# Optimization experiments

Measured on AMD Instinct MI355X. Metric: run time of the kernel, lower is better.

Reference implementation:

```python
import jax, jax.numpy as jnp
import numpy as np

B, T, D, H, V, NPOS, NDEP, OUT = 65536, 7, 100, 700, 32000, 50, 45, 93


def setup_inputs() -> dict:
    key = jax.random.key(0)
    ks = jax.random.split(key, 16)
    word_idx = jax.random.randint(ks[0], (B, T), 0, V, dtype=jnp.int64)
    drop = jax.random.uniform(ks[1], (B, T)) < 0.05
    word_idx = jnp.where(drop, -1, word_idx)
    pos_idx = jax.random.randint(ks[2], (B, T), 0, NPOS, dtype=jnp.int32)
    dep_idx = jax.random.randint(ks[3], (B, T), 0, NDEP, dtype=jnp.int32)
    s = 0.05
    return {
        "word_idx": word_idx,
        "pos_idx": pos_idx,
        "dep_idx": dep_idx,
        "word_table": jax.random.normal(ks[4], (V, D), jnp.float32) * s,
        "pos_table": jax.random.normal(ks[5], (NPOS, D), jnp.float32) * s,
        "dep_table": jax.random.normal(ks[6], (NDEP, D), jnp.float32) * s,
        "Ww": jax.random.normal(ks[7], (T * D, H), jnp.float32) * s,
        "bw": jax.random.normal(ks[8], (H,), jnp.float32) * s,
        "Wp": jax.random.normal(ks[9], (T * D, H), jnp.float32) * s,
        "bp": jax.random.normal(ks[10], (H,), jnp.float32) * s,
        "Wd": jax.random.normal(ks[11], (T * D, H), jnp.float32) * s,
        "bd": jax.random.normal(ks[12], (H,), jnp.float32) * s,
        "Wo": jax.random.normal(ks[13], (H, OUT), jnp.float32) * s,
        "bo": jax.random.normal(ks[14], (OUT,), jnp.float32) * s,
    }


def reference(word_idx, pos_idx, dep_idx, word_table, pos_table, dep_table,
              Ww, bw, Wp, bp, Wd, bd, Wo, bo):
    b = word_idx.shape[0]
    # word lookup with -1 -> zeros (the '_' token), batched gather instead of
    # per-token loop + serial torch.cat
    we = jnp.where((word_idx >= 0)[..., None],
                   word_table[jnp.clip(word_idx, 0)], 0.0)          # [B,T,D]
    we = we.reshape(b, -1)                                           # [B,700]
    pe = pos_table[pos_idx].reshape(b, -1)                           # [B,700]
    de = dep_table[dep_idx].reshape(b, -1)                           # [B,700]
    h = (we @ Ww + bw) + (pe @ Wp + bp) + (de @ Wd + bd)             # [B,700]
    h = h * h * h                                                    # torch.pow(., 3)
    logits = h @ Wo + bo                                             # [B,OUT]
    # original applies Softmax(dim=0) to a 1-D [OUT] vector per example;
    # batched equivalent is softmax over the class axis
    return jax.nn.softmax(logits, axis=-1)
```

## Files before the change

kernel.cpp:

```cpp
#include <hip/hip_runtime.h>
#include <hip/hip_bf16.h>
#include <stdint.h>

#define T_ 7
#define D_ 100
#define KP 704
#define KSTEPS 22
#define NP 704
#define NT 44
#define BM 64
#define OUTC 93
#define OUTP 96
#define NT2 6
#define NPOS 50
#define NDEP 45

typedef __attribute__((ext_vector_type(8))) short bf16x8;
typedef __attribute__((ext_vector_type(4))) float f32x4;

#define SZ_WWP (22*44*64*8*2)
#define O_WWP  0
#define O_WOP  (O_WWP + SZ_WWP)
#define SZ_WOP (22*6*64*8*2)
#define O_PTB  (O_WOP + SZ_WOP)
#define SZ_PTB (7*50*704*2)
#define O_DTB  (O_PTB + SZ_PTB)
#define SZ_DTB (7*45*704*2)
#define O_HB   (O_DTB + SZ_DTB)

__device__ __forceinline__ unsigned short f2bf(float f) {
  unsigned u = __float_as_uint(f);
  u += 0x7FFFu + ((u >> 16) & 1u);
  return (unsigned short)(u >> 16);
}
__device__ __forceinline__ float bf2f(unsigned short h) {
  return __uint_as_float(((unsigned)h) << 16);
}
__device__ __forceinline__ void addbf8(float* s, const uint4 v) {
  unsigned u0 = v.x, u1 = v.y, u2 = v.z, u3 = v.w;
  s[0] += __uint_as_float(u0 << 16);
  s[1] += __uint_as_float(u0 & 0xFFFF0000u);
  s[2] += __uint_as_float(u1 << 16);
  s[3] += __uint_as_float(u1 & 0xFFFF0000u);
  s[4] += __uint_as_float(u2 << 16);
  s[5] += __uint_as_float(u2 & 0xFFFF0000u);
  s[6] += __uint_as_float(u3 << 16);
  s[7] += __uint_as_float(u3 & 0xFFFF0000u);
}

__global__ void pack_w(const float* __restrict__ W, unsigned short* __restrict__ out,
                       int Ksrc, int Nsrc, int ntiles) {
  int blk = blockIdx.x;
  int ks = blk / ntiles, nt = blk - ks*ntiles;
  int l = threadIdx.x;
  int n = nt*16 + (l & 15);
  int k0 = ks*32 + (l >> 4)*8;
  unsigned short v[8];
#pragma unroll
  for (int j = 0; j < 8; ++j) {
    int k = k0 + j;
    float f = (k < Ksrc && n < Nsrc) ? W[k*Nsrc + n] : 0.f;
    v[j] = f2bf(f);
  }
  ((uint4*)out)[blk*64 + l] = *(const uint4*)v;
}

__global__ void pack_tbl(const float* __restrict__ tbl, const float* __restrict__ W,
                         unsigned short* __restrict__ out, int P, int total) {
  int id = blockIdx.x*256 + threadIdx.x;
  if (id >= total) return;
  int hp = id % 704;
  int tp = id / 704;
  int p = tp % P, t = tp / P;
  float acc = 0.f;
  if (hp < 700) {
    const float* tr = tbl + p*100;
    const float* wc = W + t*100*700 + hp;
#pragma unroll 4
    for (int d = 0; d < 100; ++d) acc += tr[d] * wc[d*700];
  }
  out[id] = f2bf(acc);
}

__global__ void bias_sum(const float* __restrict__ a, const float* __restrict__ b,
                         const float* __restrict__ c, float* __restrict__ o) {
  int i = blockIdx.x*256 + threadIdx.x;
  if (i < 704) o[i] = (i < 700) ? (a[i] + b[i] + c[i]) : 0.f;
}

struct SMem {
  union {
    struct { unsigned short A[2][4*64*8]; unsigned short Bb[2][44*64*8]; } mm;
    struct { unsigned short h3[64*712]; float logits[64*96]; } ep;
  } u;
  int widx[64][8];
  int pidxs[64][8];
  int didxs[64][8];
  float bo_l[96];
};

__launch_bounds__(512, 2)
__global__ void dp_main(const int* __restrict__ word_idx,
                        const int* __restrict__ pos_idx,
                        const int* __restrict__ dep_idx,
                        const float* __restrict__ word_table,
                        const unsigned short* __restrict__ WwP,
                        const unsigned short* __restrict__ WoP,
                        const unsigned short* __restrict__ PTb,
                        const unsigned short* __restrict__ DTb,
                        const float* __restrict__ hbias,
                        const float* __restrict__ bo,
                        float* __restrict__ out) {
  __shared__ SMem sm;
  const int tid = threadIdx.x;
  const int lane = tid & 63;
  const int w = tid >> 6;
  const int blockRow = blockIdx.x * BM;

  if (tid < 448) {
    int r = tid / 7, t = tid - r*7;
    int g = (blockRow + r)*7 + t;
    sm.widx[r][t]  = word_idx[g];
    sm.pidxs[r][t] = pos_idx[g];
    sm.didxs[r][t] = dep_idx[g];
  }
  if (tid < 96) sm.bo_l[tid] = (tid < OUTC) ? bo[tid] : 0.f;

  f32x4 acc0[11], acc1[11];
#pragma unroll
  for (int j = 0; j < 11; ++j) { acc0[j] = (f32x4){0,0,0,0}; acc1[j] = (f32x4){0,0,0,0}; }

  __syncthreads();

  auto issueB = [&](int ks, int buf) {
    const unsigned short* src = WwP + (size_t)ks*(44*64*8);
    unsigned short* dst = sm.u.mm.Bb[buf];
#pragma unroll
    for (int it = 0; it < 6; ++it) {
      int slot = it*512 + tid;
      if (slot < 44*64) {
        __builtin_amdgcn_global_load_lds(
            (const __attribute__((address_space(1))) unsigned int*)(src + slot*8),
            (__attribute__((address_space(3))) unsigned int*)(dst + slot*8),
            16, 0, 0);
      }
    }
  };
  auto gatherA = [&](int ks, float4& fa, float4& fb) {
    int mt = tid >> 6;
    int l = tid & 63;
    int row = mt*16 + (l & 15);
    int k0 = ks*32 + (l >> 4)*8;
    int t0 = k0 / 100, d0 = k0 - t0*100;
    fa = make_float4(0.f,0.f,0.f,0.f);
    fb = make_float4(0.f,0.f,0.f,0.f);
    {
      int wi = sm.widx[row][t0];
      if (wi >= 0) fa = *(const float4*)(word_table + (size_t)wi*100 + d0);
    }
    int k4 = k0 + 4; int t1 = k4 / 100, d1 = k4 - t1*100;
    if (t1 < 7) {
      int wi = sm.widx[row][t1];
      if (wi >= 0) fb = *(const float4*)(word_table + (size_t)wi*100 + d1);
    }
  };
  auto writeA = [&](int buf, float4 fa, float4 fb) {
    unsigned short v[8];
    v[0]=f2bf(fa.x); v[1]=f2bf(fa.y); v[2]=f2bf(fa.z); v[3]=f2bf(fa.w);
    v[4]=f2bf(fb.x); v[5]=f2bf(fb.y); v[6]=f2bf(fb.z); v[7]=f2bf(fb.w);
    ((uint4*)sm.u.mm.A[buf])[tid] = *(const uint4*)v;
  };
  const int mtb = (w >> 2) * 2;
  const int ntb = (w & 3) * 11;
  auto compute = [&](int buf) {
    const bf16x8* Af = (const bf16x8*)sm.u.mm.A[buf];
    const bf16x8* Bf = (const bf16x8*)sm.u.mm.Bb[buf];
    bf16x8 a0 = Af[(mtb + 0)*64 + lane];
    bf16x8 a1 = Af[(mtb + 1)*64 + lane];
#pragma unroll
    for (int j = 0; j < 11; ++j) {
      bf16x8 b = Bf[(ntb + j)*64 + lane];
      acc0[j] = __builtin_amdgcn_mfma_f32_16x16x32_bf16(a0, b, acc0[j], 0, 0, 0);
      acc1[j] = __builtin_amdgcn_mfma_f32_16x16x32_bf16(a1, b, acc1[j], 0, 0, 0);
    }
  };

  issueB(0, 0);
  if (tid < 256) {
    float4 fa, fb;
    gatherA(0, fa, fb);
    writeA(0, fa, fb);
  }
  __syncthreads();

  int buf = 0;
  for (int ks = 0; ks < KSTEPS; ++ks) {
    float4 na, nb;
    const bool pre = (ks + 1 < KSTEPS);
    if (pre) {
      issueB(ks + 1, buf ^ 1);
      if (tid < 256) gatherA(ks + 1, na, nb);
    }
    compute(buf);
    if (pre && tid < 256) writeA(buf ^ 1, na, nb);
    __syncthreads();
    buf ^= 1;
  }

  {
    unsigned short* h3 = sm.u.ep.h3;
#pragma unroll 1
    for (int it = 0; it < 11; ++it) {
      int v = it*512 + tid;
      int row = v / 88;
      int c8 = v - row*88;
      int cb = c8*8;
      float s0[8];
      float4 hb0 = *(const float4*)(hbias + cb);
      float4 hb1 = *(const float4*)(hbias + cb + 4);
      s0[0]=hb0.x; s0[1]=hb0.y; s0[2]=hb0.z; s0[3]=hb0.w;
      s0[4]=hb1.x; s0[5]=hb1.y; s0[6]=hb1.z; s0[7]=hb1.w;
#pragma unroll
      for (int t = 0; t < 7; ++t) {
        int p = sm.pidxs[row][t];
        addbf8(s0, *(const uint4*)(PTb + ((size_t)(t*NPOS + p))*704 + cb));
        int dd = sm.didxs[row][t];
        addbf8(s0, *(const uint4*)(DTb + ((size_t)(t*NDEP + dd))*704 + cb));
      }
      unsigned short o[8];
#pragma unroll
      for (int j = 0; j < 8; ++j) o[j] = f2bf(s0[j]);
      *(uint4*)(h3 + row*712 + cb) = *(const uint4*)o;
    }
  }
  __syncthreads();

  {
    unsigned short* h3 = sm.u.ep.h3;
    const int lr = (lane >> 4)*4, lc = lane & 15;
#pragma unroll
    for (int j = 0; j < 11; ++j) {
      int col = (ntb + j)*16 + lc;
      {
        int rb = (mtb + 0)*16 + lr;
#pragma unroll
        for (int r = 0; r < 4; ++r) {
          int off = (rb + r)*712 + col;
          float h = acc0[j][r] + bf2f(h3[off]);
          h3[off] = f2bf(h*h*h);
        }
      }
      {
        int rb = (mtb + 1)*16 + lr;
#pragma unroll
        for (int r = 0; r < 4; ++r) {
          int off = (rb + r)*712 + col;
          float h = acc1[j][r] + bf2f(h3[off]);
          h3[off] = f2bf(h*h*h);
        }
      }
    }
  }
  __syncthreads();

  {
    const unsigned short* h3 = sm.u.ep.h3;
    int mt = w >> 1;
    int nb2 = (w & 1)*3;
    f32x4 c2[3];
#pragma unroll
    for (int jn = 0; jn < 3; ++jn) c2[jn] = (f32x4){0,0,0,0};
    const bf16x8* WoF = (const bf16x8*)WoP;
    bf16x8 bfr[3];
#pragma unroll
    for (int jn = 0; jn < 3; ++jn) bfr[jn] = WoF[(size_t)(nb2 + jn)*64 + lane];
    const int arow = mt*16 + (lane & 15);
    const int koff = (lane >> 4)*8;
    for (int ks = 0; ks < KSTEPS; ++ks) {
      bf16x8 a = *(const bf16x8*)(h3 + arow*712 + ks*32 + koff);
      bf16x8 bn[3];
      if (ks < KSTEPS-1) {
#pragma unroll
        for (int jn = 0; jn < 3; ++jn) bn[jn] = WoF[((size_t)(ks+1)*6 + nb2 + jn)*64 + lane];
      }
#pragma unroll
      for (int jn = 0; jn < 3; ++jn)
        c2[jn] = __builtin_amdgcn_mfma_f32_16x16x32_bf16(a, bfr[jn], c2[jn], 0, 0, 0);
      if (ks < KSTEPS-1) {
#pragma unroll
        for (int jn = 0; jn < 3; ++jn) bfr[jn] = bn[jn];
      }
    }
    float* lg = sm.u.ep.logits;
    const int lr = (lane >> 4)*4, lc = lane & 15;
#pragma unroll
    for (int jn = 0; jn < 3; ++jn)
#pragma unroll
      for (int r = 0; r < 4; ++r)
        lg[(mt*16 + lr + r)*96 + (nb2 + jn)*16 + lc] = c2[jn][r];
  }
  __syncthreads();

  {
    const float* lg = sm.u.ep.logits;
    int row = tid >> 3, s = tid & 7;
    const float4* lp = (const float4*)(lg + row*96 + s*12);
    float4 xa = lp[0], xb = lp[1], xc = lp[2];
    float x[12] = {xa.x,xa.y,xa.z,xa.w, xb.x,xb.y,xb.z,xb.w, xc.x,xc.y,xc.z,xc.w};
    int cb = s*12;
    float mx = -1e30f;
#pragma unroll
    for (int i = 0; i < 12; ++i) {
      int c = cb + i;
      x[i] += sm.bo_l[c];
      mx = fmaxf(mx, (c < OUTC) ? x[i] : -1e30f);
    }
    mx = fmaxf(mx, __shfl_xor(mx, 1, 8));
    mx = fmaxf(mx, __shfl_xor(mx, 2, 8));
    mx = fmaxf(mx, __shfl_xor(mx, 4, 8));
    float e[12]; float sum = 0.f;
#pragma unroll
    for (int i = 0; i < 12; ++i) {
      int c = cb + i;
      e[i] = (c < OUTC) ? __expf(x[i] - mx) : 0.f;
      sum += e[i];
    }
    sum += __shfl_xor(sum, 1, 8);
    sum += __shfl_xor(sum, 2, 8);
    sum += __shfl_xor(sum, 4, 8);
    float inv = 1.0f / sum;
    float* op = out + (size_t)(blockRow + row)*OUTC;
#pragma unroll
    for (int i = 0; i < 12; ++i) {
      int c = cb + i;
      if (c < OUTC) op[c] = e[i]*inv;
    }
  }
}

extern "C" void kernel_launch(void* const* d_in, const int* in_sizes, int n_in,
                              void* d_out, int out_size, void* d_ws, size_t ws_size,
                              hipStream_t stream) {
  const int*   word_idx   = (const int*)d_in[0];
  const int*   pos_idx    = (const int*)d_in[1];
  const int*   dep_idx    = (const int*)d_in[2];
  const float* word_table = (const float*)d_in[3];
  const float* pos_table  = (const float*)d_in[4];
  const float* dep_table  = (const float*)d_in[5];
  const float* Ww = (const float*)d_in[6];
  const float* bw = (const float*)d_in[7];
  const float* Wp = (const float*)d_in[8];
  const float* bp = (const float*)d_in[9];
  const float* Wd = (const float*)d_in[10];
  const float* bd = (const float*)d_in[11];
  const float* Wo = (const float*)d_in[12];
  const float* bo = (const float*)d_in[13];
  float* out = (float*)d_out;

  char* ws = (char*)d_ws;
  unsigned short* WwP   = (unsigned short*)(ws + O_WWP);
  unsigned short* WoP   = (unsigned short*)(ws + O_WOP);
  unsigned short* PTb   = (unsigned short*)(ws + O_PTB);
  unsigned short* DTb   = (unsigned short*)(ws + O_DTB);
  float*          hbias = (float*)(ws + O_HB);

  pack_w<<<22*44, 64, 0, stream>>>(Ww, WwP, 700, 700, 44);
  pack_w<<<22*6,  64, 0, stream>>>(Wo, WoP, 700, OUTC, 6);
  pack_tbl<<<(7*50*704 + 255)/256, 256, 0, stream>>>(pos_table, Wp, PTb, 50, 7*50*704);
  pack_tbl<<<(7*45*704 + 255)/256, 256, 0, stream>>>(dep_table, Wd, DTb, 45, 7*45*704);
  bias_sum<<<3, 256, 0, stream>>>(bw, bp, bd, hbias);
  dp_main<<<65536/BM, 512, 0, stream>>>(word_idx, pos_idx, dep_idx, word_table,
                                        WwP, WoP, PTb, DTb, hbias, bo, out);
}
```

Baseline: 307.2 us.

## Fold pos/dep tables and bias into one-hot extended GEMM K dimension

Adds the pos/dep lookups and the bias to the main GEMM as one-hot columns. K grows from 704 to 1376, and a concatenated weight matrix is built that holds Ww, the precomputed table×W products and a bias row. This removes the separate bf16 gather-add epilogue. It also switches to single-buffered LDS with two barriers per step, shrinks the h3 buffer by processing the second GEMM in two column halves, compacts index storage, and raises launch bounds to 4 blocks per CU. The cost is nearly double the MFMA work in the first GEMM and less overlap of loads with compute.

Result: slower. 333.2 us (+8.4%).

```diff
diff --git a/kernel.cpp b/kernel.cpp
--- a/kernel.cpp
+++ b/kernel.cpp
@@ -1,51 +1,26 @@
 #include <hip/hip_runtime.h>
-#include <hip/hip_bf16.h>
 #include <stdint.h>
 
-#define T_ 7
-#define D_ 100
-#define KP 704
-#define KSTEPS 22
-#define NP 704
-#define NT 44
 #define BM 64
+#define NTT 44
+#define KSTEPS 43
+#define KE 1376
+#define H3S 360
 #define OUTC 93
-#define OUTP 96
-#define NT2 6
-#define NPOS 50
-#define NDEP 45
+#define KS2 22
 
 typedef __attribute__((ext_vector_type(8))) short bf16x8;
 typedef __attribute__((ext_vector_type(4))) float f32x4;
 
-#define SZ_WWP (22*44*64*8*2)
-#define O_WWP  0
-#define O_WOP  (O_WWP + SZ_WWP)
-#define SZ_WOP (22*6*64*8*2)
-#define O_PTB  (O_WOP + SZ_WOP)
-#define SZ_PTB (7*50*704*2)
-#define O_DTB  (O_PTB + SZ_PTB)
-#define SZ_DTB (7*45*704*2)
-#define O_HB   (O_DTB + SZ_DTB)
+#define O_WB   0
+#define SZ_WB  (KSTEPS*NTT*64*8*2)
+#define O_WOP  (O_WB + SZ_WB)
+#define SZ_WOP (KS2*6*64*8*2)
 
 __device__ __forceinline__ unsigned short f2bf(float f) {
   unsigned u = __float_as_uint(f);
   u += 0x7FFFu + ((u >> 16) & 1u);
   return (unsigned short)(u >> 16);
-}
-__device__ __forceinline__ float bf2f(unsigned short h) {
-  return __uint_as_float(((unsigned)h) << 16);
-}
-__device__ __forceinline__ void addbf8(float* s, const uint4 v) {
-  unsigned u0 = v.x, u1 = v.y, u2 = v.z, u3 = v.w;
-  s[0] += __uint_as_float(u0 << 16);
-  s[1] += __uint_as_float(u0 & 0xFFFF0000u);
-  s[2] += __uint_as_float(u1 << 16);
-  s[3] += __uint_as_float(u1 & 0xFFFF0000u);
-  s[4] += __uint_as_float(u2 << 16);
-  s[5] += __uint_as_float(u2 & 0xFFFF0000u);
-  s[6] += __uint_as_float(u3 << 16);
-  s[7] += __uint_as_float(u3 & 0xFFFF0000u);
 }
 
 __global__ void pack_w(const float* __restrict__ W, unsigned short* __restrict__ out,
@@ -54,7 +29,7 @@
   int ks = blk / ntiles, nt = blk - ks*ntiles;
   int l = threadIdx.x;
   int n = nt*16 + (l & 15);
-  int k0 = ks*32 + (l >> 4)*8;
+  int k0 = ks*32 + ((l >> 4) << 3);
   unsigned short v[8];
 #pragma unroll
   for (int j = 0; j < 8; ++j) {
@@ -65,50 +40,68 @@
   ((uint4*)out)[blk*64 + l] = *(const uint4*)v;
 }
 
-__global__ void pack_tbl(const float* __restrict__ tbl, const float* __restrict__ W,
-                         unsigned short* __restrict__ out, int P, int total) {
-  int id = blockIdx.x*256 + threadIdx.x;
-  if (id >= total) return;
-  int hp = id % 704;
-  int tp = id / 704;
-  int p = tp % P, t = tp / P;
-  float acc = 0.f;
-  if (hp < 700) {
-    const float* tr = tbl + p*100;
-    const float* wc = W + t*100*700 + hp;
+__global__ void build_WB(const float* __restrict__ Ww, const float* __restrict__ Wp,
+                         const float* __restrict__ Wd, const float* __restrict__ pos_table,
+                         const float* __restrict__ dep_table, const float* __restrict__ bw,
+                         const float* __restrict__ bp, const float* __restrict__ bd,
+                         unsigned short* __restrict__ out) {
+  int blk = blockIdx.x;
+  int ks = blk / 11, q = blk - ks*11;
+  int l = threadIdx.x & 63;
+  int nt = q*4 + (threadIdx.x >> 6);
+  int n = nt*16 + (l & 15);
+  int k0 = ks*32 + ((l >> 4) << 3);
+  unsigned short v[8];
+#pragma unroll
+  for (int j = 0; j < 8; ++j) {
+    int k = k0 + j;
+    float val = 0.f;
+    if (n < 700) {
+      if (k < 700) {
+        val = Ww[k*700 + n];
+      } else if (k < 1050) {
+        int u = k - 700; int t = u/50; int p = u - t*50;
+        const float* tr = pos_table + p*100;
+        const float* wc = Wp + (t*100)*700 + n;
+        float a = 0.f;
 #pragma unroll 4
-    for (int d = 0; d < 100; ++d) acc += tr[d] * wc[d*700];
-  }
-  out[id] = f2bf(acc);
-}
-
-__global__ void bias_sum(const float* __restrict__ a, const float* __restrict__ b,
-                         const float* __restrict__ c, float* __restrict__ o) {
-  int i = blockIdx.x*256 + threadIdx.x;
-  if (i < 704) o[i] = (i < 700) ? (a[i] + b[i] + c[i]) : 0.f;
+        for (int d = 0; d < 100; ++d) a += tr[d] * wc[d*700];
+        val = a;
+      } else if (k < 1365) {
+        int u = k - 1050; int t = u/45; int dd = u - t*45;
+        const float* tr = dep_table + dd*100;
+        const float* wc = Wd + (t*100)*700 + n;
+        float a = 0.f;
+#pragma unroll 4
+        for (int d = 0; d < 100; ++d) a += tr[d] * wc[d*700];
+        val = a;
+      } else if (k == 1365) {
+        val = bw[n] + bp[n] + bd[n];
+      }
+    }
+    v[j] = f2bf(val);
+  }
+  ((uint4*)out)[(ks*NTT + nt)*64 + l] = *(const uint4*)v;
 }
 
 struct SMem {
   union {
-    struct { unsigned short A[2][4*64*8]; unsigned short Bb[2][44*64*8]; } mm;
-    struct { unsigned short h3[64*712]; float logits[64*96]; } ep;
+    struct { unsigned short A[4*64*8]; unsigned short B[NTT*64*8]; } mm;
+    unsigned short h3h[64*H3S];
   } u;
-  int widx[64][8];
-  int pidxs[64][8];
-  int didxs[64][8];
+  unsigned short widx[64][8];
+  unsigned char  pidx[64][8];
+  unsigned char  didx[64][8];
   float bo_l[96];
 };
 
-__launch_bounds__(512, 2)
+__launch_bounds__(512, 4)
 __global__ void dp_main(const int* __restrict__ word_idx,
                         const int* __restrict__ pos_idx,
                         const int* __restrict__ dep_idx,
                         const float* __restrict__ word_table,
-                        const unsigned short* __restrict__ WwP,
+                        const unsigned short* __restrict__ WB,
                         const unsigned short* __restrict__ WoP,
-                        const unsigned short* __restrict__ PTb,
-                        const unsigned short* __restrict__ DTb,
-                        const float* __restrict__ hbias,
                         const float* __restrict__ bo,
                         float* __restrict__ out) {
   __shared__ SMem sm;
@@ -120,61 +113,81 @@
   if (tid < 448) {
     int r = tid / 7, t = tid - r*7;
     int g = (blockRow + r)*7 + t;
-    sm.widx[r][t]  = word_idx[g];
-    sm.pidxs[r][t] = pos_idx[g];
-    sm.didxs[r][t] = dep_idx[g];
+    int wi = word_idx[g];
+    sm.widx[r][t] = (wi < 0) ? 0xFFFFu : (unsigned short)wi;
+    sm.pidx[r][t] = (unsigned char)pos_idx[g];
+    sm.didx[r][t] = (unsigned char)dep_idx[g];
   }
   if (tid < 96) sm.bo_l[tid] = (tid < OUTC) ? bo[tid] : 0.f;
 
+  const int amt   = tid >> 7;
+  const int alane = (tid >> 1) & 63;
+  const int ahalf = tid & 1;
+  const int arow  = amt*16 + (alane & 15);
+  const int ak    = ((alane >> 4) << 3) + ahalf*4;
+
+  const int mtb = (w >> 2) * 2;
+  const int ntb = (w & 3) * 11;
+
   f32x4 acc0[11], acc1[11];
 #pragma unroll
   for (int j = 0; j < 11; ++j) { acc0[j] = (f32x4){0,0,0,0}; acc1[j] = (f32x4){0,0,0,0}; }
 
-  __syncthreads();
-
-  auto issueB = [&](int ks, int buf) {
-    const unsigned short* src = WwP + (size_t)ks*(44*64*8);
-    unsigned short* dst = sm.u.mm.Bb[buf];
+  auto issueB = [&](int ks) {
+    const unsigned short* src = WB + (size_t)ks*(NTT*64*8);
 #pragma unroll
     for (int it = 0; it < 6; ++it) {
       int slot = it*512 + tid;
-      if (slot < 44*64) {
+      if (slot < NTT*64) {
         __builtin_amdgcn_global_load_lds(
             (const __attribute__((address_space(1))) unsigned int*)(src + slot*8),
-            (__attribute__((address_space(3))) unsigned int*)(dst + slot*8),
+            (__attribute__((address_space(3))) unsigned int*)(sm.u.mm.B + slot*8),
             16, 0, 0);
       }
     }
   };
-  auto gatherA = [&](int ks, float4& fa, float4& fb) {
-    int mt = tid >> 6;
-    int l = tid & 63;
-    int row = mt*16 + (l & 15);
-    int k0 = ks*32 + (l >> 4)*8;
-    int t0 = k0 / 100, d0 = k0 - t0*100;
-    fa = make_float4(0.f,0.f,0.f,0.f);
-    fb = make_float4(0.f,0.f,0.f,0.f);
-    {
-      int wi = sm.widx[row][t0];
-      if (wi >= 0) fa = *(const float4*)(word_table + (size_t)wi*100 + d0);
-    }
-    int k4 = k0 + 4; int t1 = k4 / 100, d1 = k4 - t1*100;
-    if (t1 < 7) {
-      int wi = sm.widx[row][t1];
-      if (wi >= 0) fb = *(const float4*)(word_table + (size_t)wi*100 + d1);
+  auto stage1 = [&](int ks, float4& g) {
+    int k0 = ks*32 + ak;
+    g = make_float4(0.f, 0.f, 0.f, 0.f);
+    if (k0 < 700) {
+      int t = k0/100, d = k0 - t*100;
+      unsigned wi = sm.widx[arow][t];
+      if (wi != 0xFFFFu) g = *(const float4*)(word_table + (size_t)wi*100 + d);
+    } else {
+      unsigned short r_[4];
+#pragma unroll
+      for (int j = 0; j < 4; ++j) {
+        int k = k0 + j;
+        unsigned short rv = 0;
+        if (k < 1050) {
+          int u = k - 700; int t = u/50; int pp = u - t*50;
+          if (pp == (int)sm.pidx[arow][t]) rv = 0x3F80;
+        } else if (k < 1365) {
+          int u = k - 1050; int t = u/45; int dd = u - t*45;
+          if (dd == (int)sm.didx[arow][t]) rv = 0x3F80;
+        } else if (k == 1365) rv = 0x3F80;
+        r_[j] = rv;
+      }
+      g.x = __uint_as_float((unsigned)r_[0] | ((unsigned)r_[1] << 16));
+      g.y = __uint_as_float((unsigned)r_[2] | ((unsigned)r_[3] << 16));
     }
   };
-  auto writeA = [&](int buf, float4 fa, float4 fb) {
-    unsigned short v[8];
-    v[0]=f2bf(fa.x); v[1]=f2bf(fa.y); v[2]=f2bf(fa.z); v[3]=f2bf(fa.w);
-    v[4]=f2bf(fb.x); v[5]=f2bf(fb.y); v[6]=f2bf(fb.z); v[7]=f2bf(fb.w);
-    ((uint4*)sm.u.mm.A[buf])[tid] = *(const uint4*)v;
+  auto stage2 = [&](int ks, float4 g) {
+    int k0 = ks*32 + ak;
+    unsigned v0, v1;
+    if (k0 < 700) {
+      v0 = (unsigned)f2bf(g.x) | ((unsigned)f2bf(g.y) << 16);
+      v1 = (unsigned)f2bf(g.z) | ((unsigned)f2bf(g.w) << 16);
+    } else {
+      v0 = __float_as_uint(g.x);
+      v1 = __float_as_uint(g.y);
+    }
+    uint2 pk; pk.x = v0; pk.y = v1;
+    *(uint2*)(sm.u.mm.A + ((amt*64 + alane)*8 + ahalf*4)) = pk;
   };
-  const int mtb = (w >> 2) * 2;
-  const int ntb = (w & 3) * 11;
-  auto compute = [&](int buf) {
-    const bf16x8* Af = (const bf16x8*)sm.u.mm.A[buf];
-    const bf16x8* Bf = (const bf16x8*)sm.u.mm.Bb[buf];
+  auto compute = [&]() {
+    const bf16x8* Af = (const bf16x8*)sm.u.mm.A;
+    const bf16x8* Bf = (const bf16x8*)sm.u.mm.B;
     bf16x8 a0 = Af[(mtb + 0)*64 + lane];
     bf16x8 a1 = Af[(mtb + 1)*64 + lane];
 #pragma unroll
@@ -185,124 +198,74 @@
     }
   };
 
-  issueB(0, 0);
-  if (tid < 256) {
-    float4 fa, fb;
-    gatherA(0, fa, fb);
-    writeA(0, fa, fb);
-  }
+  issueB(0);
   __syncthreads();
-
-  int buf = 0;
+  {
+    float4 g; stage1(0, g); stage2(0, g);
+  }
+  __syncthreads();
+
   for (int ks = 0; ks < KSTEPS; ++ks) {
-    float4 na, nb;
+    float4 gn;
     const bool pre = (ks + 1 < KSTEPS);
-    if (pre) {
-      issueB(ks + 1, buf ^ 1);
-      if (tid < 256) gatherA(ks + 1, na, nb);
-    }
-    compute(buf);
-    if (pre && tid < 256) writeA(buf ^ 1, na, nb);
+    if (pre) stage1(ks + 1, gn);
+    compute();
     __syncthreads();
-    buf ^= 1;
+    if (pre) { issueB(ks + 1); stage2(ks + 1, gn); }
+    __syncthreads();
+  }
+
+  f32x4 c2[3];
+#pragma unroll
+  for (int jn = 0; jn < 3; ++jn) c2[jn] = (f32x4){0,0,0,0};
+  const int mt2 = w >> 1;
+  const int nb2 = (w & 1)*3;
+  const int arow2 = mt2*16 + (lane & 15);
+  const int koff2 = (lane >> 4)*8;
+  const bf16x8* WoF = (const bf16x8*)WoP;
+  const int myph = (w & 3) >> 1;
+  const int lr = ((lane >> 4) << 2), lc = lane & 15;
+
+#pragma unroll
+  for (int ph = 0; ph < 2; ++ph) {
+    if (myph == ph) {
+      int cbase = ntb*16 - ph*352;
+#pragma unroll
+      for (int j = 0; j < 11; ++j) {
+#pragma unroll
+        for (int r = 0; r < 4; ++r) {
+          float h0 = acc0[j][r];
+          float h1 = acc1[j][r];
+          sm.u.h3h[((mtb+0)*16 + lr + r)*H3S + cbase + j*16 + lc] = f2bf(h0*h0*h0);
+          sm.u.h3h[((mtb+1)*16 + lr + r)*H3S + cbase + j*16 + lc] = f2bf(h1*h1*h1);
+        }
+      }
+    }
+    __syncthreads();
+#pragma unroll 2
+    for (int ksl = 0; ksl < 11; ++ksl) {
+      bf16x8 a = *(const bf16x8*)(sm.u.h3h + arow2*H3S + ksl*32 + koff2);
+      int ks2 = ph*11 + ksl;
+#pragma unroll
+      for (int jn = 0; jn < 3; ++jn) {
+        bf16x8 b = WoF[(size_t)(ks2*6 + nb2 + jn)*64 + lane];
+        c2[jn] = __builtin_amdgcn_mfma_f32_16x16x32_bf16(a, b, c2[jn], 0, 0, 0);
+      }
+    }
+    __syncthreads();
   }
 
   {
-    unsigned short* h3 = sm.u.ep.h3;
-#pragma unroll 1
-    for (int it = 0; it < 11; ++it) {
-      int v = it*512 + tid;
-      int row = v / 88;
-      int c8 = v - row*88;
-      int cb = c8*8;
-      float s0[8];
-      float4 hb0 = *(const float4*)(hbias + cb);
-      float4 hb1 = *(const float4*)(hbias + cb + 4);
-      s0[0]=hb0.x; s0[1]=hb0.y; s0[2]=hb0.z; s0[3]=hb0.w;
-      s0[4]=hb1.x; s0[5]=hb1.y; s0[6]=hb1.z; s0[7]=hb1.w;
-#pragma unroll
-      for (int t = 0; t < 7; ++t) {
-        int p = sm.pidxs[row][t];
-        addbf8(s0, *(const uint4*)(PTb + ((size_t)(t*NPOS + p))*704 + cb));
-        int dd = sm.didxs[row][t];
-        addbf8(s0, *(const uint4*)(DTb + ((size_t)(t*NDEP + dd))*704 + cb));
-      }
-      unsigned short o[8];
-#pragma unroll
-      for (int j = 0; j < 8; ++j) o[j] = f2bf(s0[j]);
-      *(uint4*)(h3 + row*712 + cb) = *(const uint4*)o;
-    }
+    float* lg = (float*)sm.u.h3h;
+#pragma unroll
+    for (int jn = 0; jn < 3; ++jn)
+#pragma unroll
+      for (int r = 0; r < 4; ++r)
+        lg[(mt2*16 + lr + r)*96 + (nb2 + jn)*16 + lc] = c2[jn][r];
   }
   __syncthreads();
-
   {
-    unsigned short* h3 = sm.u.ep.h3;
-    const int lr = (lane >> 4)*4, lc = lane & 15;
-#pragma unroll
-    for (int j = 0; j < 11; ++j) {
-      int col = (ntb + j)*16 + lc;
-      {
-        int rb = (mtb + 0)*16 + lr;
-#pragma unroll
-        for (int r = 0; r < 4; ++r) {
-          int off = (rb + r)*712 + col;
-          float h = acc0[j][r] + bf2f(h3[off]);
-          h3[off] = f2bf(h*h*h);
-        }
-      }
-      {
-        int rb = (mtb + 1)*16 + lr;
-#pragma unroll
-        for (int r = 0; r < 4; ++r) {
-          int off = (rb + r)*712 + col;
-          float h = acc1[j][r] + bf2f(h3[off]);
-          h3[off] = f2bf(h*h*h);
-        }
-      }
-    }
-  }
-  __syncthreads();
-
-  {
-    const unsigned short* h3 = sm.u.ep.h3;
-    int mt = w >> 1;
-    int nb2 = (w & 1)*3;
-    f32x4 c2[3];
-#pragma unroll
-    for (int jn = 0; jn < 3; ++jn) c2[jn] = (f32x4){0,0,0,0};
-    const bf16x8* WoF = (const bf16x8*)WoP;
-    bf16x8 bfr[3];
-#pragma unroll
-    for (int jn = 0; jn < 3; ++jn) bfr[jn] = WoF[(size_t)(nb2 + jn)*64 + lane];
-    const int arow = mt*16 + (lane & 15);
-    const int koff = (lane >> 4)*8;
-    for (int ks = 0; ks < KSTEPS; ++ks) {
-      bf16x8 a = *(const bf16x8*)(h3 + arow*712 + ks*32 + koff);
-      bf16x8 bn[3];
-      if (ks < KSTEPS-1) {
-#pragma unroll
-        for (int jn = 0; jn < 3; ++jn) bn[jn] = WoF[((size_t)(ks+1)*6 + nb2 + jn)*64 + lane];
-      }
-#pragma unroll
-      for (int jn = 0; jn < 3; ++jn)
-        c2[jn] = __builtin_amdgcn_mfma_f32_16x16x32_bf16(a, bfr[jn], c2[jn], 0, 0, 0);
-      if (ks < KSTEPS-1) {
-#pragma unroll
-        for (int jn = 0; jn < 3; ++jn) bfr[jn] = bn[jn];
-      }
-    }
-    float* lg = sm.u.ep.logits;
-    const int lr = (lane >> 4)*4, lc = lane & 15;
-#pragma unroll
-    for (int jn = 0; jn < 3; ++jn)
-#pragma unroll
-      for (int r = 0; r < 4; ++r)
-        lg[(mt*16 + lr + r)*96 + (nb2 + jn)*16 + lc] = c2[jn][r];
-  }
-  __syncthreads();
-
-  {
-    const float* lg = sm.u.ep.logits;
+    const float* lg = (const float*)sm.u.h3h;
     int row = tid >> 3, s = tid & 7;
     const float4* lp = (const float4*)(lg + row*96 + s*12);
     float4 xa = lp[0], xb = lp[1], xc = lp[2];
@@ -358,17 +321,11 @@
   float* out = (float*)d_out;
 
   char* ws = (char*)d_ws;
-  unsigned short* WwP   = (unsigned short*)(ws + O_WWP);
-  unsigned short* WoP   = (unsigned short*)(ws + O_WOP);
-  unsigned short* PTb   = (unsigned short*)(ws + O_PTB);
-  unsigned short* DTb   = (unsigned short*)(ws + O_DTB);
-  float*          hbias = (float*)(ws + O_HB);
-
-  pack_w<<<22*44, 64, 0, stream>>>(Ww, WwP, 700, 700, 44);
-  pack_w<<<22*6,  64, 0, stream>>>(Wo, WoP, 700, OUTC, 6);
-  pack_tbl<<<(7*50*704 + 255)/256, 256, 0, stream>>>(pos_table, Wp, PTb, 50, 7*50*704);
-  pack_tbl<<<(7*45*704 + 255)/256, 256, 0, stream>>>(dep_table, Wd, DTb, 45, 7*45*704);
-  bias_sum<<<3, 256, 0, stream>>>(bw, bp, bd, hbias);
+  unsigned short* WBp = (unsigned short*)(ws + O_WB);
+  unsigned short* WoP = (unsigned short*)(ws + O_WOP);
+
+  build_WB<<<KSTEPS*11, 256, 0, stream>>>(Ww, Wp, Wd, pos_table, dep_table, bw, bp, bd, WBp);
+  pack_w<<<KS2*6, 64, 0, stream>>>(Wo, WoP, 700, OUTC, 6);
   dp_main<<<65536/BM, 512, 0, stream>>>(word_idx, pos_idx, dep_idx, word_table,
-                                        WwP, WoP, PTb, DTb, hbias, bo, out);
-}
+                                        WBp, WoP, bo, out);
+}
```

## Split fused kernel into large-tile word GEMM and separate logits/softmax kernel

Applied to the files above, without the earlier changes.

Replaces the single fused kernel with two kernels when workspace allows. The first runs the word-embedding GEMM with 256x176 tiles and 1024 threads, writing bf16 hidden pre-activations to a 65536x704 workspace buffer. The second adds the pos/dep lookup contributions and bias, cubes, and runs the output GEMM and softmax in a chunked pipeline with small shared memory so more blocks fit per CU. This trades roughly 180 MB of extra global write and read traffic for better weight reuse and occupancy. The old fused kernel stays as a fallback.

New measurement: 866.3 us. +182.0%, slower.

```diff
diff --git a/kernel.cpp b/kernel.cpp
--- a/kernel.cpp
+++ b/kernel.cpp
@@ -1,32 +1,33 @@
 #include <hip/hip_runtime.h>
-#include <hip/hip_bf16.h>
 #include <stdint.h>
 
-#define T_ 7
-#define D_ 100
-#define KP 704
-#define KSTEPS 22
-#define NP 704
-#define NT 44
-#define BM 64
 #define OUTC 93
-#define OUTP 96
-#define NT2 6
+#define KS1 22
 #define NPOS 50
 #define NDEP 45
+#define BM1 256
+#define BN1 176
+#define NTL 11
+#define BMF 64
+#define H3SF 360
 
 typedef __attribute__((ext_vector_type(8))) short bf16x8;
 typedef __attribute__((ext_vector_type(4))) float f32x4;
-
-#define SZ_WWP (22*44*64*8*2)
+typedef __attribute__((ext_vector_type(4))) float fvec4;
+
 #define O_WWP  0
+#define SZ_WWP (KS1*44*64*8*2)
 #define O_WOP  (O_WWP + SZ_WWP)
-#define SZ_WOP (22*6*64*8*2)
+#define SZ_WOP (KS1*6*64*8*2)
 #define O_PTB  (O_WOP + SZ_WOP)
-#define SZ_PTB (7*50*704*2)
+#define SZ_PTB (7*NPOS*704*2)
 #define O_DTB  (O_PTB + SZ_PTB)
-#define SZ_DTB (7*45*704*2)
+#define SZ_DTB (7*NDEP*704*2)
 #define O_HB   (O_DTB + SZ_DTB)
+#define SZ_HB  (704*4)
+#define O_HW   (O_HB + SZ_HB)
+#define SZ_HW  ((size_t)65536*704*2)
+#define WS_NEED_SPLIT (O_HW + SZ_HW)
 
 __device__ __forceinline__ unsigned short f2bf(float f) {
   unsigned u = __float_as_uint(f);
@@ -54,7 +55,7 @@
   int ks = blk / ntiles, nt = blk - ks*ntiles;
   int l = threadIdx.x;
   int n = nt*16 + (l & 15);
-  int k0 = ks*32 + (l >> 4)*8;
+  int k0 = ks*32 + ((l >> 4) << 3);
   unsigned short v[8];
 #pragma unroll
   for (int j = 0; j < 8; ++j) {
@@ -88,7 +89,257 @@
   if (i < 704) o[i] = (i < 700) ? (a[i] + b[i] + c[i]) : 0.f;
 }
 
-struct SMem {
+struct SM1 {
+  unsigned short A[2][16*64*8];
+  unsigned short B[2][NTL*64*8];
+  unsigned short widx[BM1][8];
+};
+
+__launch_bounds__(1024, 4)
+__global__ void gemm_hw(const int* __restrict__ word_idx,
+                        const float* __restrict__ word_table,
+                        const unsigned short* __restrict__ WwP,
+                        unsigned short* __restrict__ hw) {
+  __shared__ SM1 sm;
+  const int tid = threadIdx.x;
+  const int lane = tid & 63;
+  const int w = tid >> 6;
+
+  int D = blockIdx.x;
+  int g = (D & 7)*128 + (D >> 3);
+  const int nb = g & 3;
+  const int mb = g >> 2;
+  const int rowbase = mb * BM1;
+
+#pragma unroll
+  for (int i = tid; i < BM1*8; i += 1024) {
+    int r = i >> 3, c = i & 7;
+    unsigned short v = 0xFFFFu;
+    if (c < 7) {
+      int wi = word_idx[(size_t)(rowbase + r)*7 + c];
+      v = (wi < 0) ? 0xFFFFu : (unsigned short)wi;
+    }
+    sm.widx[r][c] = v;
+  }
+
+  const int amt  = tid >> 6;
+  const int al   = tid & 63;
+  const int arow = amt*16 + (al & 15);
+  const int akq  = (al >> 4) << 3;
+
+  f32x4 acc[NTL];
+#pragma unroll
+  for (int j = 0; j < NTL; ++j) acc[j] = (f32x4){0,0,0,0};
+
+  auto issueB = [&](int ks, int bb) {
+    const unsigned short* src = WwP + ((size_t)(ks*44 + nb*NTL))*64*8;
+    unsigned short* dst = sm.B[bb];
+    if (tid < NTL*64) {
+      __builtin_amdgcn_global_load_lds(
+          (const __attribute__((address_space(1))) unsigned int*)(src + tid*8),
+          (__attribute__((address_space(3))) unsigned int*)(dst + tid*8),
+          16, 0, 0);
+    }
+  };
+  auto stage1 = [&](int ks, fvec4& fa, fvec4& fb) {
+    int k0 = ks*32 + akq;
+    fa = (fvec4){0,0,0,0};
+    fb = (fvec4){0,0,0,0};
+    int t0 = k0/100, d0 = k0 - t0*100;
+    unsigned wi0 = sm.widx[arow][t0];
+    if (wi0 != 0xFFFFu)
+      fa = *(const fvec4*)(word_table + (size_t)wi0*100 + d0);
+    int k4 = k0 + 4;
+    int t1 = k4/100, d1 = k4 - t1*100;
+    unsigned wi1 = sm.widx[arow][t1];
+    if (wi1 != 0xFFFFu)
+      fb = *(const fvec4*)(word_table + (size_t)wi1*100 + d1);
+  };
+  auto stage2 = [&](fvec4 fa, fvec4 fb, int ab) {
+    uint4 pk;
+    pk.x = (unsigned)f2bf(fa[0]) | ((unsigned)f2bf(fa[1]) << 16);
+    pk.y = (unsigned)f2bf(fa[2]) | ((unsigned)f2bf(fa[3]) << 16);
+    pk.z = (unsigned)f2bf(fb[0]) | ((unsigned)f2bf(fb[1]) << 16);
+    pk.w = (unsigned)f2bf(fb[2]) | ((unsigned)f2bf(fb[3]) << 16);
+    ((uint4*)sm.A[ab])[tid] = pk;
+  };
+  auto compute = [&](int bb) {
+    const bf16x8* Af = (const bf16x8*)sm.A[bb];
+    const bf16x8* Bf = (const bf16x8*)sm.B[bb];
+    bf16x8 a = Af[w*64 + lane];
+#pragma unroll
+    for (int j = 0; j < NTL; ++j) {
+      bf16x8 b = Bf[j*64 + lane];
+      acc[j] = __builtin_amdgcn_mfma_f32_16x16x32_bf16(a, b, acc[j], 0, 0, 0);
+    }
+  };
+
+  issueB(0, 0);
+  __syncthreads();
+  { fvec4 fa, fb; stage1(0, fa, fb); stage2(fa, fb, 0); }
+  __syncthreads();
+
+  int buf = 0;
+  for (int ks = 0; ks < KS1; ++ks) {
+    const bool pre = (ks + 1 < KS1);
+    fvec4 fa, fb;
+    if (pre) { issueB(ks + 1, buf ^ 1); stage1(ks + 1, fa, fb); }
+    compute(buf);
+    if (pre) stage2(fa, fb, buf ^ 1);
+    __syncthreads();
+    buf ^= 1;
+  }
+
+  const int lr = (lane >> 4) << 2;
+  const int lc = lane & 15;
+#pragma unroll
+  for (int j = 0; j < NTL; ++j) {
+#pragma unroll
+    for (int r = 0; r < 4; ++r) {
+      size_t row = (size_t)rowbase + w*16 + lr + r;
+      int col = nb*BN1 + j*16 + lc;
+      __builtin_nontemporal_store(f2bf(acc[j][r]), hw + row*704 + col);
+    }
+  }
+}
+
+struct SM2 {
+  union { unsigned short h3[64*72]; float lg[64*96]; } u;
+  unsigned char pidx[64][8];
+  unsigned char didx[64][8];
+  float bo_l[96];
+};
+
+__launch_bounds__(512, 6)
+__global__ void logits_sm(const int* __restrict__ pos_idx,
+                          const int* __restrict__ dep_idx,
+                          const unsigned short* __restrict__ hw,
+                          const unsigned short* __restrict__ PTb,
+                          const unsigned short* __restrict__ DTb,
+                          const float* __restrict__ hbias,
+                          const unsigned short* __restrict__ WoP,
+                          const float* __restrict__ bo,
+                          float* __restrict__ out) {
+  __shared__ SM2 sm;
+  const int tid = threadIdx.x;
+  const int lane = tid & 63;
+  const int w = tid >> 6;
+  const int blockRow = blockIdx.x * 64;
+
+  if (tid < 448) {
+    int r = tid / 7, t = tid - r*7;
+    size_t gidx = (size_t)(blockRow + r)*7 + t;
+    sm.pidx[r][t] = (unsigned char)pos_idx[gidx];
+    sm.didx[r][t] = (unsigned char)dep_idx[gidx];
+  }
+  if (tid < 96) sm.bo_l[tid] = (tid < OUTC) ? bo[tid] : 0.f;
+
+  f32x4 c2[3];
+#pragma unroll
+  for (int jn = 0; jn < 3; ++jn) c2[jn] = (f32x4){0,0,0,0};
+  const int mt2 = w >> 1;
+  const int nb2 = (w & 1)*3;
+  const bf16x8* WoF = (const bf16x8*)WoP;
+  const int r2  = tid >> 3;
+  const int seg = tid & 7;
+
+  __syncthreads();
+
+  for (int c = 0; c < 11; ++c) {
+    int col = c*64 + seg*8;
+    uint4 hwv = *(const uint4*)(hw + (size_t)(blockRow + r2)*704 + col);
+    float s[8];
+    {
+      float4 hb0 = *(const float4*)(hbias + col);
+      float4 hb1 = *(const float4*)(hbias + col + 4);
+      s[0]=hb0.x; s[1]=hb0.y; s[2]=hb0.z; s[3]=hb0.w;
+      s[4]=hb1.x; s[5]=hb1.y; s[6]=hb1.z; s[7]=hb1.w;
+    }
+#pragma unroll
+    for (int t = 0; t < 7; ++t) {
+      int p = sm.pidx[r2][t];
+      addbf8(s, *(const uint4*)(PTb + ((size_t)(t*NPOS + p))*704 + col));
+      int dd = sm.didx[r2][t];
+      addbf8(s, *(const uint4*)(DTb + ((size_t)(t*NDEP + dd))*704 + col));
+    }
+    unsigned short o8[8];
+    {
+      float hv[8];
+      hv[0]=s[0]+bf2f((unsigned short)(hwv.x & 0xFFFF));
+      hv[1]=s[1]+bf2f((unsigned short)(hwv.x >> 16));
+      hv[2]=s[2]+bf2f((unsigned short)(hwv.y & 0xFFFF));
+      hv[3]=s[3]+bf2f((unsigned short)(hwv.y >> 16));
+      hv[4]=s[4]+bf2f((unsigned short)(hwv.z & 0xFFFF));
+      hv[5]=s[5]+bf2f((unsigned short)(hwv.z >> 16));
+      hv[6]=s[6]+bf2f((unsigned short)(hwv.w & 0xFFFF));
+      hv[7]=s[7]+bf2f((unsigned short)(hwv.w >> 16));
+#pragma unroll
+      for (int i = 0; i < 8; ++i) { float h = hv[i]; o8[i] = f2bf(h*h*h); }
+    }
+    *(uint4*)(sm.u.h3 + r2*72 + seg*8) = *(const uint4*)o8;
+    __syncthreads();
+
+#pragma unroll
+    for (int ksl = 0; ksl < 2; ++ksl) {
+      bf16x8 a = *(const bf16x8*)(sm.u.h3 + (mt2*16 + (lane & 15))*72 + ksl*32 + ((lane >> 4) << 3));
+      int ks2 = c*2 + ksl;
+#pragma unroll
+      for (int jn = 0; jn < 3; ++jn) {
+        bf16x8 b = WoF[(size_t)(ks2*6 + nb2 + jn)*64 + lane];
+        c2[jn] = __builtin_amdgcn_mfma_f32_16x16x32_bf16(a, b, c2[jn], 0, 0, 0);
+      }
+    }
+    __syncthreads();
+  }
+
+  {
+    float* lg = sm.u.lg;
+    const int lr = ((lane >> 4) << 2), lc = lane & 15;
+#pragma unroll
+    for (int jn = 0; jn < 3; ++jn)
+#pragma unroll
+      for (int r = 0; r < 4; ++r)
+        lg[(mt2*16 + lr + r)*96 + (nb2 + jn)*16 + lc] = c2[jn][r];
+  }
+  __syncthreads();
+  {
+    const float* lg = sm.u.lg;
+    int row = tid >> 3, sgl = tid & 7;
+    const float4* lp = (const float4*)(lg + row*96 + sgl*12);
+    float4 xa = lp[0], xb = lp[1], xc = lp[2];
+    float x[12] = {xa.x,xa.y,xa.z,xa.w, xb.x,xb.y,xb.z,xb.w, xc.x,xc.y,xc.z,xc.w};
+    int cb = sgl*12;
+    float mx = -1e30f;
+#pragma unroll
+    for (int i = 0; i < 12; ++i) {
+      int cc = cb + i;
+      x[i] += sm.bo_l[cc];
+      mx = fmaxf(mx, (cc < OUTC) ? x[i] : -1e30f);
+    }
+    mx = fmaxf(mx, __shfl_xor(mx, 1, 8));
+    mx = fmaxf(mx, __shfl_xor(mx, 2, 8));
+    mx = fmaxf(mx, __shfl_xor(mx, 4, 8));
+    float e[12]; float sum = 0.f;
+#pragma unroll
+    for (int i = 0; i < 12; ++i) {
+      int cc = cb + i;
+      e[i] = (cc < OUTC) ? __expf(x[i] - mx) : 0.f;
+      sum += e[i];
+    }
+    sum += __shfl_xor(sum, 1, 8);
+    sum += __shfl_xor(sum, 2, 8);
+    sum += __shfl_xor(sum, 4, 8);
+    float inv = 1.0f / sum;
+    float* op = out + (size_t)(blockRow + row)*OUTC;
+#pragma unroll
+    for (int i = 0; i < 12; ++i) {
+      int cc = cb + i;
+      if (cc < OUTC) __builtin_nontemporal_store(e[i]*inv, op + cc);
+    }
+  }
+}
+
+struct SMF {
   union {
     struct { unsigned short A[2][4*64*8]; unsigned short Bb[2][44*64*8]; } mm;
     struct { unsigned short h3[64*712]; float logits[64*96]; } ep;
@@ -100,22 +351,22 @@
 };
 
 __launch_bounds__(512, 2)
-__global__ void dp_main(const int* __restrict__ word_idx,
-                        const int* __restrict__ pos_idx,
-                        const int* __restrict__ dep_idx,
-                        const float* __restrict__ word_table,
-                        const unsigned short* __restrict__ WwP,
-                        const unsigned short* __restrict__ WoP,
-                        const unsigned short* __restrict__ PTb,
-                        const unsigned short* __restrict__ DTb,
-                        const float* __restrict__ hbias,
-                        const float* __restrict__ bo,
-                        float* __restrict__ out) {
-  __shared__ SMem sm;
+__global__ void dp_fused(const int* __restrict__ word_idx,
+                         const int* __restrict__ pos_idx,
+                         const int* __restrict__ dep_idx,
+                         const float* __restrict__ word_table,
+                         const unsigned short* __restrict__ WwP,
+                         const unsigned short* __restrict__ WoP,
+                         const unsigned short* __restrict__ PTb,
+                         const unsigned short* __restrict__ DTb,
+                         const float* __restrict__ hbias,
+                         const float* __restrict__ bo,
+                         float* __restrict__ out) {
+  __shared__ SMF sm;
   const int tid = threadIdx.x;
   const int lane = tid & 63;
   const int w = tid >> 6;
-  const int blockRow = blockIdx.x * BM;
+  const int blockRow = blockIdx.x * BMF;
 
   if (tid < 448) {
     int r = tid / 7, t = tid - r*7;
@@ -194,9 +445,9 @@
   __syncthreads();
 
   int buf = 0;
-  for (int ks = 0; ks < KSTEPS; ++ks) {
+  for (int ks = 0; ks < KS1; ++ks) {
     float4 na, nb;
-    const bool pre = (ks + 1 < KSTEPS);
+    const bool pre = (ks + 1 < KS1);
     if (pre) {
       issueB(ks + 1, buf ^ 1);
       if (tid < 256) gatherA(ks + 1, na, nb);
@@ -276,17 +527,17 @@
     for (int jn = 0; jn < 3; ++jn) bfr[jn] = WoF[(size_t)(nb2 + jn)*64 + lane];
     const int arow = mt*16 + (lane & 15);
     const int koff = (lane >> 4)*8;
-    for (int ks = 0; ks < KSTEPS; ++ks) {
+    for (int ks = 0; ks < KS1; ++ks) {
       bf16x8 a = *(const bf16x8*)(h3 + arow*712 + ks*32 + koff);
       bf16x8 bn[3];
-      if (ks < KSTEPS-1) {
+      if (ks < KS1-1) {
 #pragma unroll
         for (int jn = 0; jn < 3; ++jn) bn[jn] = WoF[((size_t)(ks+1)*6 + nb2 + jn)*64 + lane];
       }
 #pragma unroll
       for (int jn = 0; jn < 3; ++jn)
         c2[jn] = __builtin_amdgcn_mfma_f32_16x16x32_bf16(a, bfr[jn], c2[jn], 0, 0, 0);
-      if (ks < KSTEPS-1) {
+      if (ks < KS1-1) {
 #pragma unroll
         for (int jn = 0; jn < 3; ++jn) bfr[jn] = bn[jn];
       }
@@ -363,12 +614,19 @@
   unsigned short* PTb   = (unsigned short*)(ws + O_PTB);
   unsigned short* DTb   = (unsigned short*)(ws + O_DTB);
   float*          hbias = (float*)(ws + O_HB);
-
-  pack_w<<<22*44, 64, 0, stream>>>(Ww, WwP, 700, 700, 44);
-  pack_w<<<22*6,  64, 0, stream>>>(Wo, WoP, 700, OUTC, 6);
-  pack_tbl<<<(7*50*704 + 255)/256, 256, 0, stream>>>(pos_table, Wp, PTb, 50, 7*50*704);
-  pack_tbl<<<(7*45*704 + 255)/256, 256, 0, stream>>>(dep_table, Wd, DTb, 45, 7*45*704);
+  unsigned short* hw    = (unsigned short*)(ws + O_HW);
+
+  pack_w<<<KS1*44, 64, 0, stream>>>(Ww, WwP, 700, 700, 44);
+  pack_w<<<KS1*6,  64, 0, stream>>>(Wo, WoP, 700, OUTC, 6);
+  pack_tbl<<<(7*NPOS*704 + 255)/256, 256, 0, stream>>>(pos_table, Wp, PTb, NPOS, 7*NPOS*704);
+  pack_tbl<<<(7*NDEP*704 + 255)/256, 256, 0, stream>>>(dep_table, Wd, DTb, NDEP, 7*NDEP*704);
   bias_sum<<<3, 256, 0, stream>>>(bw, bp, bd, hbias);
-  dp_main<<<65536/BM, 512, 0, stream>>>(word_idx, pos_idx, dep_idx, word_table,
-                                        WwP, WoP, PTb, DTb, hbias, bo, out);
-}
+
+  if (ws_size >= WS_NEED_SPLIT) {
+    gemm_hw<<<1024, 1024, 0, stream>>>(word_idx, word_table, WwP, hw);
+    logits_sm<<<1024, 512, 0, stream>>>(pos_idx, dep_idx, hw, PTb, DTb, hbias, WoP, bo, out);
+  } else {
+    dp_fused<<<65536/BMF, 512, 0, stream>>>(word_idx, pos_idx, dep_idx, word_table,
+                                            WwP, WoP, PTb, DTb, hbias, bo, out);
+  }
+}
```
